# Kernel optimization log

Hardware: AMD Instinct MI355X
Metric: run time of the kernel (lower is better)

Reference implementation:

```python
import jax, jax.numpy as jnp
import numpy as np

N = 100000   # num nodes
E = 600000   # num edges
H = 128      # hidden dim
R = 8        # num relations
B = 4        # num bases


def setup_inputs() -> dict:
    key = jax.random.key(0)
    ks = jax.random.split(key, 12)
    return {
        "node_ids": jnp.arange(N, dtype=jnp.int64 if jax.config.jax_enable_x64 else jnp.int32),
        "src": jax.random.randint(ks[0], (E,), 0, N),
        "dst": jax.random.randint(ks[1], (E,), 0, N),
        "etype": jax.random.randint(ks[2], (E,), 0, R),
        "embedding": jax.random.normal(ks[3], (N, H), dtype=jnp.float32),
        "V1": jax.random.normal(ks[4], (B, H, H), dtype=jnp.float32) * 0.05,
        "comp1": jax.random.normal(ks[5], (R, B), dtype=jnp.float32),
        "loop1": jax.random.normal(ks[6], (H, H), dtype=jnp.float32) * 0.05,
        "bias1": jax.random.normal(ks[7], (H,), dtype=jnp.float32) * 0.05,
        "V2": jax.random.normal(ks[8], (B, H, H), dtype=jnp.float32) * 0.05,
        "comp2": jax.random.normal(ks[9], (R, B), dtype=jnp.float32),
        "loop2": jax.random.normal(ks[10], (H, H), dtype=jnp.float32) * 0.05,
        "bias2": jax.random.normal(ks[11], (H,), dtype=jnp.float32) * 0.05,
    }


def _rgcn_layer(h, src, dst, etype, V, comp, loopW, bias, activate):
    # basis decomposition: W_r = sum_b comp[r,b] * V[b]   -> [R, in, out]
    W = jnp.einsum('rb,bio->rio', comp, V)
    # transform all nodes under all relations once (avoids per-edge GEMM): [N, R, out]
    hw = jnp.einsum('ni,rio->nro', h, W)
    # gather per-edge message for its (src, relation): [E, out]
    m = hw[src, etype]
    # scatter-sum aggregation at destination nodes
    agg = jax.ops.segment_sum(m, dst, num_segments=h.shape[0])
    out = agg + bias + h @ loopW  # bias + self-loop
    return jax.nn.relu(out) if activate else out


def reference(node_ids, src, dst, etype, embedding,
              V1, comp1, loop1, bias1,
              V2, comp2, loop2, bias2):
    h = embedding[node_ids]                       # EmbeddingLayer
    h = _rgcn_layer(h, src, dst, etype, V1, comp1, loop1, bias1, activate=True)
    h = _rgcn_layer(h, src, dst, etype, V2, comp2, loop2, bias2, activate=False)
    return h
```

## Files before the change

kernel.cpp:

```cpp
#include <hip/hip_runtime.h>
#include <hip/hip_bf16.h>

#define NN 100000
#define NE 600000
#define HH 128
#define NB 4
#define TILE 2048
#define NTILES ((NN + TILE - 1) / TILE)

typedef __attribute__((ext_vector_type(8))) short bf16x8;
typedef __attribute__((ext_vector_type(4))) float f32x4;
typedef __attribute__((ext_vector_type(4))) float vfloat4;
typedef __attribute__((ext_vector_type(4))) unsigned short ushort4v;

static __device__ __forceinline__ short f2bf(float f) {
  unsigned u = __float_as_uint(f);
  unsigned r = (u + 0x7fffu + ((u >> 16) & 1u)) >> 16;
  return (short)r;
}

static __device__ __forceinline__ float bf2f(short s) {
  unsigned u = (unsigned)(unsigned short)s;
  return __uint_as_float(u << 16);
}

__global__ __launch_bounds__(256) void build_wt(const float* __restrict__ V,
                                                const float* __restrict__ loopW,
                                                short* __restrict__ W8)
{
  int idx = blockIdx.x * blockDim.x + threadIdx.x;
  int j  = idx & 7;
  int o  = (idx >> 3) & 127;
  int kb = idx >> 10;
  int k  = kb * 8 + j;
  float v;
  if (k < 512) v = V[(size_t)k * HH + o];
  else         v = loopW[(size_t)(k - 512) * HH + o];
  W8[idx] = f2bf(v);
}

__global__ __launch_bounds__(256) void cast_h(const float* __restrict__ in,
                                              short* __restrict__ out)
{
  const int n8 = NN * HH / 8;
  for (int i = blockIdx.x * blockDim.x + threadIdx.x; i < n8; i += gridDim.x * blockDim.x) {
    const vfloat4* p = reinterpret_cast<const vfloat4*>(in + i * 8);
    vfloat4 a = p[0], b = p[1];
    bf16x8 o;
#pragma unroll
    for (int j = 0; j < 4; ++j) { o[j] = f2bf(a[j]); o[j + 4] = f2bf(b[j]); }
    reinterpret_cast<bf16x8*>(out)[i] = o;
  }
}


__global__ __launch_bounds__(256) void hist_deg(const int* __restrict__ dst,
                                                int* __restrict__ deg)
{
  int e = blockIdx.x * blockDim.x + threadIdx.x;
  if (e < NE) atomicAdd(&deg[dst[e]], 1);
}

__global__ __launch_bounds__(256) void scan_tiles(const int* __restrict__ deg,
                                                  int* __restrict__ tilesum)
{
  __shared__ int red[256];
  const int tid = threadIdx.x;
  int base = blockIdx.x * TILE + tid * 8;
  int s = 0;
#pragma unroll
  for (int j = 0; j < 8; ++j) {
    int i = base + j;
    if (i < NN) s += deg[i];
  }
  red[tid] = s;
  __syncthreads();
  for (int off = 128; off > 0; off >>= 1) {
    if (tid < off) red[tid] += red[tid + off];
    __syncthreads();
  }
  if (tid == 0) tilesum[blockIdx.x] = red[0];
}

__global__ __launch_bounds__(256) void scan_final(const int* deg,
                                                  const int* __restrict__ tilesum,
                                                  int* __restrict__ rowptr,
                                                  int* cursor)
{
  __shared__ int lds[256];
  const int tid = threadIdx.x;
  int pre = 0;
  for (int t = 0; t < NTILES; ++t)
    if (t < blockIdx.x) pre += tilesum[t];

  int base = blockIdx.x * TILE + tid * 8;
  int d[8];
  int s = 0;
#pragma unroll
  for (int j = 0; j < 8; ++j) {
    int i = base + j;
    d[j] = (i < NN) ? deg[i] : 0;
    s += d[j];
  }
  lds[tid] = s;
  __syncthreads();
  for (int off = 1; off < 256; off <<= 1) {
    int t = (tid >= off) ? lds[tid - off] : 0;
    __syncthreads();
    lds[tid] += t;
    __syncthreads();
  }
  int run = pre + lds[tid] - s;
#pragma unroll
  for (int j = 0; j < 8; ++j) {
    int i = base + j;
    if (i < NN) {
      rowptr[i] = run;
      cursor[i] = run;
      run += d[j];
    }
  }
  if (blockIdx.x == NTILES - 1 && tid == 255)
    rowptr[NN] = pre + lds[255];
}

__global__ __launch_bounds__(256) void scatter_edges(
    const int* __restrict__ src, const int* __restrict__ dst, const int* __restrict__ ety,
    int* __restrict__ cursor, int* __restrict__ csr)
{
  int e = blockIdx.x * blockDim.x + threadIdx.x;
  if (e >= NE) return;
  int d = dst[e];
  int p = atomicAdd(&cursor[d], 1);
  csr[p] = src[e] | (ety[e] << 20);
}

template<int FINAL>
__global__ __launch_bounds__(512, 6) void rgcn_fused(
    const int* __restrict__ rowptr, const int* __restrict__ csr,
    const float* __restrict__ comp,
    const short* __restrict__ hbf,
    const short* __restrict__ W8,
    const float* __restrict__ bias,
    short* __restrict__ outH,
    float* __restrict__ outF)
{
  __shared__ bf16x8 gl[32][64];
  __shared__ bf16x8 wl[2][512];

  const int tid  = threadIdx.x;
  const int wave = tid >> 6;
  const int lane = tid & 63;
  const int b  = lane >> 4;
  const int q  = lane & 15;
  const int base = blockIdx.x * 32;

  const int mt = wave >> 2;
  const int ct0 = (wave & 3) * 2;
  const int mynode = base + mt * 16 + q;

  const bf16x8* wsrc = reinterpret_cast<const bf16x8*>(W8);
  bf16x8 w0reg = wsrc[tid];

#pragma unroll 1
  for (int pp = 0; pp < 2; ++pp) {
    const int row0 = wave * 4 + pp * 2;
    const int row1 = row0 + 1;
    int       i0 = __builtin_amdgcn_readfirstlane(rowptr[base + row0]);
    const int E0 = __builtin_amdgcn_readfirstlane(rowptr[base + row0 + 1]);
    int       i1 = E0;
    const int E1 = __builtin_amdgcn_readfirstlane(rowptr[base + row1 + 1]);

    float a0[8] = {0.f, 0.f, 0.f, 0.f, 0.f, 0.f, 0.f, 0.f};
    float a1[8] = {0.f, 0.f, 0.f, 0.f, 0.f, 0.f, 0.f, 0.f};

    while (i0 < E0 || i1 < E1) {
      const bool d0 = i0 < E0, d1 = i1 < E1;
      bf16x8 H[8];
      float  C[8];
      if (d0) {
#pragma unroll
        for (int j = 0; j < 4; ++j) {
          const int idx = i0 + j;
          const bool v = idx < E0;
          const int e = csr[v ? idx : E0 - 1];
          H[j] = reinterpret_cast<const bf16x8*>(hbf + (size_t)(e & 0xFFFFF) * HH)[q];
          C[j] = v ? comp[(e >> 20) * NB + b] : 0.f;
        }
      }
      if (d1) {
#pragma unroll
        for (int j = 0; j < 4; ++j) {
          const int idx = i1 + j;
          const bool v = idx < E1;
          const int e = csr[v ? idx : E1 - 1];
          H[4 + j] = reinterpret_cast<const bf16x8*>(hbf + (size_t)(e & 0xFFFFF) * HH)[q];
          C[4 + j] = v ? comp[(e >> 20) * NB + b] : 0.f;
        }
      }
      if (d0) {
#pragma unroll
        for (int j = 0; j < 4; ++j)
#pragma unroll
          for (int k = 0; k < 8; ++k) a0[k] += bf2f(H[j][k]) * C[j];
        i0 += 4;
      }
      if (d1) {
#pragma unroll
        for (int j = 0; j < 4; ++j)
#pragma unroll
          for (int k = 0; k < 8; ++k) a1[k] += bf2f(H[4 + j][k]) * C[4 + j];
        i1 += 4;
      }
    }

    bf16x8 o0, o1;
#pragma unroll
    for (int j = 0; j < 8; ++j) { o0[j] = f2bf(a0[j]); o1[j] = f2bf(a1[j]); }
    gl[row0][lane ^ (row0 & 7)] = o0;
    gl[row1][lane ^ (row1 & 7)] = o1;
  }

  const bf16x8* ha = reinterpret_cast<const bf16x8*>(hbf + (size_t)mynode * HH);
  bf16x8 hreg[4];
#pragma unroll
  for (int j = 0; j < 4; ++j) hreg[j] = ha[j * 4 + b];

  wl[0][tid] = w0reg;
  __syncthreads();

  const int r  = q;
  const int g8 = b;

  f32x4 acc0 = {0.f, 0.f, 0.f, 0.f};
  f32x4 acc1 = {0.f, 0.f, 0.f, 0.f};

#pragma unroll 1
  for (int ks = 0; ks < 20; ++ks) {
    const int cur = ks & 1;
    bf16x8 nxt;
    if (ks < 19) nxt = wsrc[(ks + 1) * 512 + tid];
    bf16x8 a = (ks < 16) ? gl[mt * 16 + r][(ks * 4 + g8) ^ (r & 7)] : hreg[ks - 16];
    bf16x8 w0 = wl[cur][g8 * 128 + (ct0 + 0) * 16 + r];
    bf16x8 w1 = wl[cur][g8 * 128 + (ct0 + 1) * 16 + r];
    acc0 = __builtin_amdgcn_mfma_f32_16x16x32_bf16(w0, a, acc0, 0, 0, 0);
    acc1 = __builtin_amdgcn_mfma_f32_16x16x32_bf16(w1, a, acc1, 0, 0, 0);
    if (ks < 19) wl[cur ^ 1][tid] = nxt;
    __syncthreads();
  }

  if (FINAL) {
    float* glf = reinterpret_cast<float*>(gl);
#pragma unroll
    for (int c = 0; c < 2; ++c) {
      const f32x4 acc = c ? acc1 : acc0;
      const int row = mt * 16 + r;
      const int o = (ct0 + c) * 16 + g8 * 4;
      vfloat4 bs = *reinterpret_cast<const vfloat4*>(bias + o);
      vfloat4 x;
#pragma unroll
      for (int rr = 0; rr < 4; ++rr) x[rr] = acc[rr] + bs[rr];
      const int s = (ct0 + c) * 4 + g8;
      const int phys = s ^ (row & 7);
      *reinterpret_cast<vfloat4*>(glf + row * 128 + phys * 4) = x;
    }
    __syncthreads();
#pragma unroll
    for (int p = 0; p < 2; ++p) {
      const int flat = p * 512 + tid;
      const int row = flat >> 5, s = flat & 31;
      const int phys = s ^ (row & 7);
      vfloat4 x = *reinterpret_cast<const vfloat4*>(glf + row * 128 + phys * 4);
      *reinterpret_cast<vfloat4*>(outF + (size_t)(base + row) * HH + s * 4) = x;
    }
  } else {
    short* glb = reinterpret_cast<short*>(gl);
#pragma unroll
    for (int c = 0; c < 2; ++c) {
      const f32x4 acc = c ? acc1 : acc0;
      const int row = mt * 16 + r;
      const int o = (ct0 + c) * 16 + g8 * 4;
      vfloat4 bs = *reinterpret_cast<const vfloat4*>(bias + o);
      ushort4v sv;
#pragma unroll
      for (int rr = 0; rr < 4; ++rr)
        sv[rr] = (unsigned short)f2bf(fmaxf(acc[rr] + bs[rr], 0.f));
      const int u8 = (ct0 + c) * 4 + g8;
      const int phys16 = (u8 >> 1) ^ (row & 7);
      *reinterpret_cast<ushort4v*>(glb + row * 128 + phys16 * 8 + (u8 & 1) * 4) = sv;
    }
    __syncthreads();
    {
      const int row = tid >> 4, s16 = tid & 15;
      const int phys = s16 ^ (row & 7);
      bf16x8 x = *reinterpret_cast<const bf16x8*>(glb + row * 128 + phys * 8);
      *reinterpret_cast<bf16x8*>(outH + (size_t)(base + row) * HH + s16 * 8) = x;
    }
  }
}

extern "C" void kernel_launch(void* const* d_in, const int* in_sizes, int n_in,
                              void* d_out, int out_size, void* d_ws, size_t ws_size,
                              hipStream_t stream)
{
  const int*   srcp  = (const int*)d_in[1];
  const int*   dstp  = (const int*)d_in[2];
  const int*   etp   = (const int*)d_in[3];
  const float* emb   = (const float*)d_in[4];
  const float* V1    = (const float*)d_in[5];
  const float* comp1 = (const float*)d_in[6];
  const float* loop1 = (const float*)d_in[7];
  const float* bias1 = (const float*)d_in[8];
  const float* V2    = (const float*)d_in[9];
  const float* comp2 = (const float*)d_in[10];
  const float* loop2 = (const float*)d_in[11];
  const float* bias2 = (const float*)d_in[12];
  float* out = (float*)d_out;

  char* ws = (char*)d_ws;
  short* Wt1     = (short*)(ws);
  short* Wt2     = (short*)(ws + 163840);
  short* hbf1    = (short*)(ws + 327680);
  short* hbf2    = (short*)(ws + 25927680);
  int*   deg     = (int*)  (ws + 51527680);
  int*   rowptr  = (int*)  (ws + 51927680);
  int*   csr     = (int*)  (ws + 52327696);
  int*   tilesum = (int*)  (ws + 54727696);

  const int fused_blocks = NN / 32;
  const int e_blocks     = (NE + 255) / 256;

  hipMemsetAsync(deg, 0, NN * sizeof(int), stream);
  hipLaunchKernelGGL(hist_deg, dim3(e_blocks), dim3(256), 0, stream, dstp, deg);
  hipLaunchKernelGGL(scan_tiles, dim3(NTILES), dim3(256), 0, stream, deg, tilesum);
  hipLaunchKernelGGL(scan_final, dim3(NTILES), dim3(256), 0, stream,
                     deg, tilesum, rowptr, deg);
  hipLaunchKernelGGL(scatter_edges, dim3(e_blocks), dim3(256), 0, stream,
                     srcp, dstp, etp, deg, csr);

  hipLaunchKernelGGL(build_wt, dim3(320), dim3(256), 0, stream, V1, loop1, Wt1);
  hipLaunchKernelGGL(build_wt, dim3(320), dim3(256), 0, stream, V2, loop2, Wt2);
  hipLaunchKernelGGL(cast_h, dim3(2048), dim3(256), 0, stream, emb, hbf1);

  hipLaunchKernelGGL((rgcn_fused<0>), dim3(fused_blocks), dim3(512), 0, stream,
                     rowptr, csr, comp1, hbf1, Wt1, bias1, hbf2, (float*)nullptr);

  hipLaunchKernelGGL((rgcn_fused<1>), dim3(fused_blocks), dim3(512), 0, stream,
                     rowptr, csr, comp2, hbf2, Wt2, bias2, (short*)nullptr, out);
}
```

Measured before the change: 317.9 us.

## Single-buffer weight LDS for higher occupancy and merge prep kernels into one launch

The double-buffered weight tile in LDS becomes a single buffer, with an extra barrier before each refill, and the launch bound rises from 6 to 8 waves-per-EU so more blocks can be resident per CU. The two build_wt launches and the cast_h launch are merged into one prep_all kernel to cut launch overhead. In exchange the GEMM loop now pays two barriers per k-step instead of one, and the tighter register budget could cause spills.

```diff
diff --git a/kernel.cpp b/kernel.cpp
--- a/kernel.cpp
+++ b/kernel.cpp
@@ -24,11 +24,10 @@
   return __uint_as_float(u << 16);
 }
 
-__global__ __launch_bounds__(256) void build_wt(const float* __restrict__ V,
-                                                const float* __restrict__ loopW,
-                                                short* __restrict__ W8)
-{
-  int idx = blockIdx.x * blockDim.x + threadIdx.x;
+static __device__ __forceinline__ void build_one(const float* __restrict__ V,
+                                                 const float* __restrict__ loopW,
+                                                 short* __restrict__ W8, int idx)
+{
   int j  = idx & 7;
   int o  = (idx >> 3) & 127;
   int kb = idx >> 10;
@@ -39,17 +38,27 @@
   W8[idx] = f2bf(v);
 }
 
-__global__ __launch_bounds__(256) void cast_h(const float* __restrict__ in,
-                                              short* __restrict__ out)
-{
-  const int n8 = NN * HH / 8;
-  for (int i = blockIdx.x * blockDim.x + threadIdx.x; i < n8; i += gridDim.x * blockDim.x) {
-    const vfloat4* p = reinterpret_cast<const vfloat4*>(in + i * 8);
-    vfloat4 a = p[0], b = p[1];
-    bf16x8 o;
-#pragma unroll
-    for (int j = 0; j < 4; ++j) { o[j] = f2bf(a[j]); o[j + 4] = f2bf(b[j]); }
-    reinterpret_cast<bf16x8*>(out)[i] = o;
+__global__ __launch_bounds__(256) void prep_all(
+    const float* __restrict__ V1, const float* __restrict__ loop1, short* __restrict__ W81,
+    const float* __restrict__ V2, const float* __restrict__ loop2, short* __restrict__ W82,
+    const float* __restrict__ emb, short* __restrict__ hbf1)
+{
+  const int bid = blockIdx.x;
+  if (bid < 320) {
+    build_one(V1, loop1, W81, bid * 256 + threadIdx.x);
+  } else if (bid < 640) {
+    build_one(V2, loop2, W82, (bid - 320) * 256 + threadIdx.x);
+  } else {
+    const int n8 = NN * HH / 8;
+    int i = (bid - 640) * 256 + threadIdx.x;
+    for (; i < n8; i += 800 * 256) {
+      const vfloat4* p = reinterpret_cast<const vfloat4*>(emb + (size_t)i * 8);
+      vfloat4 a = p[0], b = p[1];
+      bf16x8 o;
+#pragma unroll
+      for (int j = 0; j < 4; ++j) { o[j] = f2bf(a[j]); o[j + 4] = f2bf(b[j]); }
+      reinterpret_cast<bf16x8*>(hbf1)[i] = o;
+    }
   }
 }
 
@@ -136,7 +145,7 @@
 }
 
 template<int FINAL>
-__global__ __launch_bounds__(512, 6) void rgcn_fused(
+__global__ __launch_bounds__(512, 8) void rgcn_fused(
     const int* __restrict__ rowptr, const int* __restrict__ csr,
     const float* __restrict__ comp,
     const short* __restrict__ hbf,
@@ -146,7 +155,7 @@
     float* __restrict__ outF)
 {
   __shared__ bf16x8 gl[32][64];
-  __shared__ bf16x8 wl[2][512];
+  __shared__ bf16x8 wl[512];
 
   const int tid  = threadIdx.x;
   const int wave = tid >> 6;
@@ -226,7 +235,7 @@
 #pragma unroll
   for (int j = 0; j < 4; ++j) hreg[j] = ha[j * 4 + b];
 
-  wl[0][tid] = w0reg;
+  wl[tid] = w0reg;
   __syncthreads();
 
   const int r  = q;
@@ -237,17 +246,20 @@
 
 #pragma unroll 1
   for (int ks = 0; ks < 20; ++ks) {
-    const int cur = ks & 1;
     bf16x8 nxt;
     if (ks < 19) nxt = wsrc[(ks + 1) * 512 + tid];
     bf16x8 a = (ks < 16) ? gl[mt * 16 + r][(ks * 4 + g8) ^ (r & 7)] : hreg[ks - 16];
-    bf16x8 w0 = wl[cur][g8 * 128 + (ct0 + 0) * 16 + r];
-    bf16x8 w1 = wl[cur][g8 * 128 + (ct0 + 1) * 16 + r];
+    bf16x8 w0 = wl[g8 * 128 + (ct0 + 0) * 16 + r];
+    bf16x8 w1 = wl[g8 * 128 + (ct0 + 1) * 16 + r];
     acc0 = __builtin_amdgcn_mfma_f32_16x16x32_bf16(w0, a, acc0, 0, 0, 0);
     acc1 = __builtin_amdgcn_mfma_f32_16x16x32_bf16(w1, a, acc1, 0, 0, 0);
-    if (ks < 19) wl[cur ^ 1][tid] = nxt;
-    __syncthreads();
-  }
+    if (ks < 19) {
+      __syncthreads();
+      wl[tid] = nxt;
+      __syncthreads();
+    }
+  }
+  __syncthreads();
 
   if (FINAL) {
     float* glf = reinterpret_cast<float*>(gl);
@@ -338,9 +350,8 @@
   hipLaunchKernelGGL(scatter_edges, dim3(e_blocks), dim3(256), 0, stream,
                      srcp, dstp, etp, deg, csr);
 
-  hipLaunchKernelGGL(build_wt, dim3(320), dim3(256), 0, stream, V1, loop1, Wt1);
-  hipLaunchKernelGGL(build_wt, dim3(320), dim3(256), 0, stream, V2, loop2, Wt2);
-  hipLaunchKernelGGL(cast_h, dim3(2048), dim3(256), 0, stream, emb, hbf1);
+  hipLaunchKernelGGL(prep_all, dim3(1440), dim3(256), 0, stream,
+                     V1, loop1, Wt1, V2, loop2, Wt2, emb, hbf1);
 
   hipLaunchKernelGGL((rgcn_fused<0>), dim3(fused_blocks), dim3(512), 0, stream,
                      rowptr, csr, comp1, hbf1, Wt1, bias1, hbf2, (float*)nullptr);
```

New measurement: 442.4 us. 1.39x slower.
